# Kernel optimization log

Measured on AMD Instinct MI355X. Metric: run time of the kernel, lower is better.

Reference implementation:

```python
import math
import jax, jax.numpy as jnp
import numpy as np

B, S, E = 4, 2048, 1024

def setup_inputs() -> dict:
    key = jax.random.key(0)
    k1, k2, k3 = jax.random.split(key, 3)
    X = jax.random.normal(k1, (B, S, E), dtype=jnp.float32)
    # nn.Linear(E, 3E): weight [3E, E], bias [3E]; scale weights for sane softmax
    W = jax.random.normal(k2, (3 * E, E), dtype=jnp.float32) * (1.0 / math.sqrt(E))
    b = jax.random.normal(k3, (3 * E,), dtype=jnp.float32) * 0.01
    return {"X": X, "W": W, "b": b}

def reference(X, W, b):
    E_ = X.shape[-1]
    # fused QKV projection: X @ W^T + b -> [B, S, 3E]
    qkv = jnp.einsum('bse,fe->bsf', X, W) + b
    q, k, v = jnp.split(qkv, 3, axis=-1)
    scores = jnp.einsum('bqe,bke->bqk', q, k) / math.sqrt(E_)
    attention_weight = jax.nn.softmax(scores, axis=-1)  # [B, S, S]
    output = jnp.einsum('bqk,bke->bqe', attention_weight, v)
    return (output, attention_weight)
```

## Files before the change

kernel.cpp:

```cpp
#include <hip/hip_runtime.h>
#include <math.h>

typedef __bf16 bf16;
typedef __bf16 bf16x4 __attribute__((ext_vector_type(4)));
typedef __bf16 bf16x8 __attribute__((ext_vector_type(8)));
typedef float f32x4 __attribute__((ext_vector_type(4)));

#define MODE_QKV    0
#define MODE_SCORES 1
#define MODE_PV     2

__device__ inline void gload_lds16(const bf16* g, bf16* l) {
    __builtin_amdgcn_global_load_lds(
        (const __attribute__((address_space(1))) void*)g,
        (__attribute__((address_space(3))) void*)l, 16, 0, 0);
}

template <int MODE>
__global__ __launch_bounds__(256) void mfma_nt(
    const bf16* __restrict__ A, const bf16* __restrict__ B,
    const float* __restrict__ bias, void* __restrict__ Cv,
    int K, int lda, int ldb, int ldc,
    long sA, long sB, long sC, float alpha)
{
    A += (long)blockIdx.z * sA;
    B += (long)blockIdx.z * sB;

    __shared__ bf16 As[128 * 32] __attribute__((aligned(16)));
    __shared__ bf16 Bs[128 * 32] __attribute__((aligned(16)));

    const int t  = threadIdx.x;
    const int m0 = blockIdx.y * 128;
    const int n0 = blockIdx.x * 128;

    const int lane = t & 63;
    const int wave = t >> 6;
    const int wrow = (wave >> 1) * 64;
    const int wcol = (wave & 1) * 64;
    const int fr   = lane & 15;
    const int kq8  = lane >> 4;

    const int r0 = t >> 2,         q0 = t & 3;
    const int r1 = (t + 256) >> 2, q1 = (t + 256) & 3;
    const int k80 = (q0 ^ ((r0 >> 1) & 3)) * 8;
    const int k81 = (q1 ^ ((r1 >> 1) & 3)) * 8;

    f32x4 acc[4][4] = {};

    for (int k0 = 0; k0 < K; k0 += 32) {
        gload_lds16(A + (long)(m0 + r0) * lda + k0 + k80, &As[t * 8]);
        gload_lds16(A + (long)(m0 + r1) * lda + k0 + k81, &As[(t + 256) * 8]);
        gload_lds16(B + (long)(n0 + r0) * ldb + k0 + k80, &Bs[t * 8]);
        gload_lds16(B + (long)(n0 + r1) * ldb + k0 + k81, &Bs[(t + 256) * 8]);
        __syncthreads();

        bf16x8 af[4], bfr[4];
#pragma unroll
        for (int i = 0; i < 4; i++) {
            const int ra = wrow + i * 16 + fr;
            const int rb = wcol + i * 16 + fr;
            af[i]  = *(const bf16x8*)&As[(ra * 4 + (kq8 ^ ((ra >> 1) & 3))) * 8];
            bfr[i] = *(const bf16x8*)&Bs[(rb * 4 + (kq8 ^ ((rb >> 1) & 3))) * 8];
        }
#pragma unroll
        for (int i = 0; i < 4; i++)
#pragma unroll
            for (int j = 0; j < 4; j++)
                acc[i][j] = __builtin_amdgcn_mfma_f32_16x16x32_bf16(
                    af[i], bfr[j], acc[i][j], 0, 0, 0);
        __syncthreads();
    }

    const int r4 = (lane >> 4) * 4;
    if constexpr (MODE == MODE_PV) {
        float* C = (float*)Cv + (long)blockIdx.z * sC;
#pragma unroll
        for (int j = 0; j < 4; j++) {
            const int col = n0 + wcol + j * 16 + fr;
#pragma unroll
            for (int i = 0; i < 4; i++)
#pragma unroll
                for (int r = 0; r < 4; r++) {
                    const long row = m0 + wrow + i * 16 + r4 + r;
                    C[row * ldc + col] = acc[i][j][r];
                }
        }
    } else {
        bf16* C = (bf16*)Cv + (long)blockIdx.z * sC;
#pragma unroll
        for (int j = 0; j < 4; j++) {
            const int col = n0 + wcol + j * 16 + fr;
            const float bv = (MODE == MODE_QKV) ? bias[col] : 0.f;
#pragma unroll
            for (int i = 0; i < 4; i++)
#pragma unroll
                for (int r = 0; r < 4; r++) {
                    const long row = m0 + wrow + i * 16 + r4 + r;
                    float v = acc[i][j][r];
                    if constexpr (MODE == MODE_QKV)
                        C[row * ldc + col] = (bf16)(v + bv);
                    else
                        C[row * ldc + col] = (bf16)__expf(alpha * v);
                }
        }
    }
}

__global__ __launch_bounds__(256) void f32_to_bf16(
    const float* __restrict__ in, bf16* __restrict__ out, long n)
{
    long i = ((long)blockIdx.x * 256 + threadIdx.x) * 4;
    if (i < n) {
        float4 v = *(const float4*)(in + i);
        bf16x4 o = { (bf16)v.x, (bf16)v.y, (bf16)v.z, (bf16)v.w };
        *(bf16x4*)(out + i) = o;
    }
}

__global__ __launch_bounds__(256) void transpose_v(
    const bf16* __restrict__ V, bf16* __restrict__ Vt)
{
    __shared__ bf16 tile[32][33];
    const bf16* Vb  = V  + (long)blockIdx.z * 2048 * 3072;
    bf16*       Vtb = Vt + (long)blockIdx.z * 1024 * 2048;
    const int s0 = blockIdx.x * 32, e0 = blockIdx.y * 32;
    const int tx = threadIdx.x & 31, ty = threadIdx.x >> 5;
#pragma unroll
    for (int i = 0; i < 32; i += 8)
        tile[ty + i][tx] = Vb[(long)(s0 + ty + i) * 3072 + e0 + tx];
    __syncthreads();
#pragma unroll
    for (int i = 0; i < 32; i += 8)
        Vtb[(long)(e0 + ty + i) * 2048 + s0 + tx] = tile[tx][ty + i];
}

__global__ __launch_bounds__(256) void norm_rows(
    bf16* __restrict__ Pu, float* __restrict__ out1)
{
    bf16* p  = Pu   + (long)blockIdx.x * 2048;
    float* o = out1 + (long)blockIdx.x * 2048;
    const int t = threadIdx.x;
    bf16x8 v = *(const bf16x8*)(p + t * 8);
    float f[8];
    float s = 0.f;
#pragma unroll
    for (int k = 0; k < 8; k++) { f[k] = (float)v[k]; s += f[k]; }
#pragma unroll
    for (int off = 32; off > 0; off >>= 1) s += __shfl_xor(s, off);
    __shared__ float red[4];
    const int wid = t >> 6, lane = t & 63;
    if (lane == 0) red[wid] = s;
    __syncthreads();
    s = red[0] + red[1] + red[2] + red[3];
    const float inv = 1.0f / s;
    float4 a, b;
    a.x = f[0] * inv; a.y = f[1] * inv; a.z = f[2] * inv; a.w = f[3] * inv;
    b.x = f[4] * inv; b.y = f[5] * inv; b.z = f[6] * inv; b.w = f[7] * inv;
    *(float4*)(o + t * 8)     = a;
    *(float4*)(o + t * 8 + 4) = b;
    bf16x8 w;
#pragma unroll
    for (int k = 0; k < 8; k++) w[k] = (bf16)(f[k] * inv);
    *(bf16x8*)(p + t * 8) = w;
}

extern "C" void kernel_launch(void* const* d_in, const int* in_sizes, int n_in,
                              void* d_out, int out_size, void* d_ws, size_t ws_size,
                              hipStream_t stream)
{
    const int B = 4, S = 2048, E = 1024;
    const float* X    = (const float*)d_in[0];
    const float* W    = (const float*)d_in[1];
    const float* bias = (const float*)d_in[2];

    float* out0 = (float*)d_out;
    float* out1 = out0 + (long)B * S * E;

    char* ws = (char*)d_ws;
    bf16* qkvb = (bf16*)(ws);
    bf16* Vt   = (bf16*)(ws + 50331648);
    bf16* Pu   = (bf16*)(ws + 67108864);
    bf16* Xb   = (bf16*)(ws + 67108864);
    bf16* Wb   = (bf16*)(ws + 83886080);

    f32_to_bf16<<<(long)B * S * E / 1024, 256, 0, stream>>>(X, Xb, (long)B * S * E);
    f32_to_bf16<<<(long)3 * E * E / 1024, 256, 0, stream>>>(W, Wb, (long)3 * E * E);

    mfma_nt<MODE_QKV><<<dim3(3 * E / 128, B * S / 128, 1), 256, 0, stream>>>(
        Xb, Wb, bias, qkvb, E, E, E, 3 * E, 0, 0, 0, 1.0f);

    transpose_v<<<dim3(S / 32, E / 32, B), 256, 0, stream>>>(qkvb + 2 * E, Vt);

    mfma_nt<MODE_SCORES><<<dim3(S / 128, S / 128, B), 256, 0, stream>>>(
        qkvb, qkvb + E, nullptr, Pu, E, 3 * E, 3 * E, S,
        (long)S * 3 * E, (long)S * 3 * E, (long)S * S, 0.03125f);

    norm_rows<<<B * S, 256, 0, stream>>>(Pu, out1);

    mfma_nt<MODE_PV><<<dim3(E / 128, S / 128, B), 256, 0, stream>>>(
        Pu, Vt, nullptr, out0, S, S, S, E,
        (long)S * S, (long)E * S, (long)S * E, 1.0f);
}
```

Before: 346.7 us.

## Triple-buffer GEMM tiles with 256x128 blocks and hand-scheduled LDS/MFMA pipeline

Reworks the shared GEMM kernel so each block computes a 256x128 tile and keeps a three-stage LDS ring buffer, issuing global-to-LDS loads two K-steps ahead. LDS reads go through inline ds_read_b128 with explicit lgkmcnt/vmcnt waits, sched barriers and setprio, so MFMAs start while later fragments are still arriving. The K loop is fully unrolled at compile time from a template trip count, with launch_bounds set for two blocks per CU. This aims to hide global and LDS latency and raise MFMA utilisation. In exchange it uses more registers (32 accumulators per thread) and more LDS, halves the grid size, and relies on fragile hand-tuned wait counts.

```diff
diff --git a/kernel.cpp b/kernel.cpp
--- a/kernel.cpp
+++ b/kernel.cpp
@@ -16,72 +16,136 @@
         (__attribute__((address_space(3))) void*)l, 16, 0, 0);
 }
 
-template <int MODE>
-__global__ __launch_bounds__(256) void mfma_nt(
+#define DSR(dst, base, imm)                                                 \
+    asm volatile("ds_read_b128 %0, %1 offset:%2"                            \
+        : "=v"(dst)                                                         \
+        : "v"((const __attribute__((address_space(3))) bf16*)(base)),       \
+          "i"(imm))
+
+#define MF(i, j) acc[i][j] = __builtin_amdgcn_mfma_f32_16x16x32_bf16(       \
+    af[i], bq[j], acc[i][j], 0, 0, 0);
+
+template <int MODE, int NT>
+__global__ __launch_bounds__(256, 2) void mfma_nt(
     const bf16* __restrict__ A, const bf16* __restrict__ B,
     const float* __restrict__ bias, void* __restrict__ Cv,
-    int K, int lda, int ldb, int ldc,
+    int lda, int ldb, int ldc,
     long sA, long sB, long sC, float alpha)
 {
     A += (long)blockIdx.z * sA;
     B += (long)blockIdx.z * sB;
 
-    __shared__ bf16 As[128 * 32] __attribute__((aligned(16)));
-    __shared__ bf16 Bs[128 * 32] __attribute__((aligned(16)));
+    __shared__ bf16 As[3 * 8192] __attribute__((aligned(16)));
+    __shared__ bf16 Bs[3 * 4096] __attribute__((aligned(16)));
 
     const int t  = threadIdx.x;
-    const int m0 = blockIdx.y * 128;
+    const int m0 = blockIdx.y * 256;
     const int n0 = blockIdx.x * 128;
 
     const int lane = t & 63;
     const int wave = t >> 6;
-    const int wrow = (wave >> 1) * 64;
-    const int wcol = (wave & 1) * 64;
+    const int wr   = (wave >> 1) * 128;
+    const int wc   = (wave & 1) * 64;
     const int fr   = lane & 15;
     const int kq8  = lane >> 4;
 
-    const int r0 = t >> 2,         q0 = t & 3;
-    const int r1 = (t + 256) >> 2, q1 = (t + 256) & 3;
-    const int k80 = (q0 ^ ((r0 >> 1) & 3)) * 8;
-    const int k81 = (q1 ^ ((r1 >> 1) & 3)) * 8;
-
-    f32x4 acc[4][4] = {};
-
-    for (int k0 = 0; k0 < K; k0 += 32) {
-        gload_lds16(A + (long)(m0 + r0) * lda + k0 + k80, &As[t * 8]);
-        gload_lds16(A + (long)(m0 + r1) * lda + k0 + k81, &As[(t + 256) * 8]);
-        gload_lds16(B + (long)(n0 + r0) * ldb + k0 + k80, &Bs[t * 8]);
-        gload_lds16(B + (long)(n0 + r1) * ldb + k0 + k81, &Bs[(t + 256) * 8]);
-        __syncthreads();
-
-        bf16x8 af[4], bfr[4];
-#pragma unroll
-        for (int i = 0; i < 4; i++) {
-            const int ra = wrow + i * 16 + fr;
-            const int rb = wcol + i * 16 + fr;
-            af[i]  = *(const bf16x8*)&As[(ra * 4 + (kq8 ^ ((ra >> 1) & 3))) * 8];
-            bfr[i] = *(const bf16x8*)&Bs[(rb * 4 + (kq8 ^ ((rb >> 1) & 3))) * 8];
-        }
-#pragma unroll
-        for (int i = 0; i < 4; i++)
-#pragma unroll
-            for (int j = 0; j < 4; j++)
-                acc[i][j] = __builtin_amdgcn_mfma_f32_16x16x32_bf16(
-                    af[i], bfr[j], acc[i][j], 0, 0, 0);
-        __syncthreads();
-    }
+    const bf16* gA0; const bf16* gA1; const bf16* gA2; const bf16* gA3;
+    const bf16* gB0; const bf16* gB1;
+    {
+        const int c0 = t,        r0 = c0 >> 2, h0 = ((c0 & 3) ^ ((r0 >> 1) & 3)) * 8;
+        const int c1 = t + 256,  r1 = c1 >> 2, h1 = ((c1 & 3) ^ ((r1 >> 1) & 3)) * 8;
+        const int c2 = t + 512,  r2 = c2 >> 2, h2 = ((c2 & 3) ^ ((r2 >> 1) & 3)) * 8;
+        const int c3 = t + 768,  r3 = c3 >> 2, h3 = ((c3 & 3) ^ ((r3 >> 1) & 3)) * 8;
+        gA0 = A + (long)(m0 + r0) * lda + h0;
+        gA1 = A + (long)(m0 + r1) * lda + h1;
+        gA2 = A + (long)(m0 + r2) * lda + h2;
+        gA3 = A + (long)(m0 + r3) * lda + h3;
+        gB0 = B + (long)(n0 + r0) * ldb + h0;
+        gB1 = B + (long)(n0 + r1) * ldb + h1;
+    }
+
+    const int swz = kq8 ^ ((fr >> 1) & 3);
+    const bf16* pA = As + (wr + fr) * 32 + swz * 8;
+    const bf16* pB = Bs + (wc + fr) * 32 + swz * 8;
+
+    f32x4 acc[8][4] = {};
+    bf16x8 af[8], bq[4];
+    int kofs = 64;
+
+#define STAGE6(SS, ko)                                                      \
+    gload_lds16(gA0 + (ko), &As[(SS) * 8192 + t * 8]);                      \
+    gload_lds16(gA1 + (ko), &As[(SS) * 8192 + (t + 256) * 8]);              \
+    gload_lds16(gA2 + (ko), &As[(SS) * 8192 + (t + 512) * 8]);              \
+    gload_lds16(gA3 + (ko), &As[(SS) * 8192 + (t + 768) * 8]);              \
+    gload_lds16(gB0 + (ko), &Bs[(SS) * 4096 + t * 8]);                      \
+    gload_lds16(gB1 + (ko), &Bs[(SS) * 4096 + (t + 256) * 8]);
+
+#define TB(CS, STG) do {                                                    \
+    if constexpr ((STG) == 1) {                                             \
+        constexpr int SS = ((CS) + 2) % 3;                                  \
+        STAGE6(SS, kofs);                                                   \
+        kofs += 32;                                                         \
+    }                                                                       \
+    DSR(af[0], pA, (CS) * 16384 + 0);                                       \
+    DSR(af[1], pA, (CS) * 16384 + 1024);                                    \
+    DSR(af[2], pA, (CS) * 16384 + 2048);                                    \
+    DSR(af[3], pA, (CS) * 16384 + 3072);                                    \
+    DSR(bq[0], pB, (CS) * 8192 + 0);                                        \
+    DSR(bq[1], pB, (CS) * 8192 + 1024);                                     \
+    DSR(bq[2], pB, (CS) * 8192 + 2048);                                     \
+    DSR(bq[3], pB, (CS) * 8192 + 3072);                                     \
+    DSR(af[4], pA, (CS) * 16384 + 4096);                                    \
+    DSR(af[5], pA, (CS) * 16384 + 5120);                                    \
+    DSR(af[6], pA, (CS) * 16384 + 6144);                                    \
+    DSR(af[7], pA, (CS) * 16384 + 7168);                                    \
+    asm volatile("s_waitcnt lgkmcnt(6)" ::: "memory");                      \
+    __builtin_amdgcn_sched_barrier(0);                                      \
+    __builtin_amdgcn_s_setprio(1);                                          \
+    MF(0,0) MF(0,1) MF(1,0) MF(1,1) MF(2,0) MF(2,1) MF(3,0) MF(3,1)         \
+    asm volatile("s_waitcnt lgkmcnt(4)" ::: "memory");                      \
+    __builtin_amdgcn_sched_barrier(0);                                      \
+    MF(0,2) MF(0,3) MF(1,2) MF(1,3) MF(2,2) MF(2,3) MF(3,2) MF(3,3)         \
+    asm volatile("s_waitcnt lgkmcnt(0)" ::: "memory");                      \
+    __builtin_amdgcn_sched_barrier(0);                                      \
+    MF(4,0) MF(4,1) MF(5,0) MF(5,1) MF(6,0) MF(6,1) MF(7,0) MF(7,1)         \
+    MF(4,2) MF(4,3) MF(5,2) MF(5,3) MF(6,2) MF(6,3) MF(7,2) MF(7,3)         \
+    __builtin_amdgcn_s_setprio(0);                                          \
+    if constexpr ((STG) == 1)                                               \
+        asm volatile("s_waitcnt vmcnt(6)" ::: "memory");                    \
+    else if constexpr ((STG) == 0)                                          \
+        asm volatile("s_waitcnt vmcnt(0)" ::: "memory");                    \
+    if constexpr ((STG) != 2) __builtin_amdgcn_s_barrier();                 \
+} while (0)
+
+    STAGE6(0, 0);
+    STAGE6(1, 32);
+    asm volatile("s_waitcnt vmcnt(6)" ::: "memory");
+    __builtin_amdgcn_s_barrier();
+
+    static_assert(NT % 3 != 0, "peel pattern assumes NT%3 in {1,2}");
+    if constexpr (NT % 3 == 2) {
+        TB(0, 1); TB(1, 1);
+        for (int g = 0; g < (NT - 5) / 3; ++g) { TB(2, 1); TB(0, 1); TB(1, 1); }
+        TB(2, 1); TB(0, 0); TB(1, 2);
+    } else {
+        TB(0, 1);
+        for (int g = 0; g < (NT - 4) / 3; ++g) { TB(1, 1); TB(2, 1); TB(0, 1); }
+        TB(1, 1); TB(2, 0); TB(0, 2);
+    }
+#undef TB
+#undef STAGE6
 
     const int r4 = (lane >> 4) * 4;
     if constexpr (MODE == MODE_PV) {
         float* C = (float*)Cv + (long)blockIdx.z * sC;
 #pragma unroll
         for (int j = 0; j < 4; j++) {
-            const int col = n0 + wcol + j * 16 + fr;
-#pragma unroll
-            for (int i = 0; i < 4; i++)
+            const int col = n0 + wc + j * 16 + fr;
+#pragma unroll
+            for (int i = 0; i < 8; i++)
 #pragma unroll
                 for (int r = 0; r < 4; r++) {
-                    const long row = m0 + wrow + i * 16 + r4 + r;
+                    const long row = m0 + wr + i * 16 + r4 + r;
                     C[row * ldc + col] = acc[i][j][r];
                 }
         }
@@ -89,13 +153,13 @@
         bf16* C = (bf16*)Cv + (long)blockIdx.z * sC;
 #pragma unroll
         for (int j = 0; j < 4; j++) {
-            const int col = n0 + wcol + j * 16 + fr;
+            const int col = n0 + wc + j * 16 + fr;
             const float bv = (MODE == MODE_QKV) ? bias[col] : 0.f;
 #pragma unroll
-            for (int i = 0; i < 4; i++)
+            for (int i = 0; i < 8; i++)
 #pragma unroll
                 for (int r = 0; r < 4; r++) {
-                    const long row = m0 + wrow + i * 16 + r4 + r;
+                    const long row = m0 + wr + i * 16 + r4 + r;
                     float v = acc[i][j][r];
                     if constexpr (MODE == MODE_QKV)
                         C[row * ldc + col] = (bf16)(v + bv);
@@ -186,18 +250,18 @@
     f32_to_bf16<<<(long)B * S * E / 1024, 256, 0, stream>>>(X, Xb, (long)B * S * E);
     f32_to_bf16<<<(long)3 * E * E / 1024, 256, 0, stream>>>(W, Wb, (long)3 * E * E);
 
-    mfma_nt<MODE_QKV><<<dim3(3 * E / 128, B * S / 128, 1), 256, 0, stream>>>(
-        Xb, Wb, bias, qkvb, E, E, E, 3 * E, 0, 0, 0, 1.0f);
+    mfma_nt<MODE_QKV, 32><<<dim3(3 * E / 128, B * S / 256, 1), 256, 0, stream>>>(
+        Xb, Wb, bias, qkvb, E, E, 3 * E, 0, 0, 0, 1.0f);
 
     transpose_v<<<dim3(S / 32, E / 32, B), 256, 0, stream>>>(qkvb + 2 * E, Vt);
 
-    mfma_nt<MODE_SCORES><<<dim3(S / 128, S / 128, B), 256, 0, stream>>>(
-        qkvb, qkvb + E, nullptr, Pu, E, 3 * E, 3 * E, S,
+    mfma_nt<MODE_SCORES, 32><<<dim3(S / 128, S / 256, B), 256, 0, stream>>>(
+        qkvb, qkvb + E, nullptr, Pu, 3 * E, 3 * E, S,
         (long)S * 3 * E, (long)S * 3 * E, (long)S * S, 0.03125f);
 
     norm_rows<<<B * S, 256, 0, stream>>>(Pu, out1);
 
-    mfma_nt<MODE_PV><<<dim3(E / 128, S / 128, B), 256, 0, stream>>>(
-        Pu, Vt, nullptr, out0, S, S, S, E,
+    mfma_nt<MODE_PV, 64><<<dim3(E / 128, S / 256, B), 256, 0, stream>>>(
+        Pu, Vt, nullptr, out0, S, S, E,
         (long)S * S, (long)E * S, (long)S * E, 1.0f);
 }
```

New measurement: 304.1 us. 12.3% less time.
